# Optimization experiments

Measured on AMD Instinct MI355X. Metric: run time of the kernel, lower is better.

The kernel has to match this reference:

```python
import jax, jax.numpy as jnp
import numpy as np

LAG = 5
MSG_HID = 256
N_ATOMS = 30
N_EDGES = N_ATOMS * (N_ATOMS - 1)  # 870
BATCH = 2
T = 200


def _rel_matrices():
    # fully-connected directed graph, no self loops (standard NRI encoding)
    recv, send = [], []
    for i in range(N_ATOMS):
        for j in range(N_ATOMS):
            if i != j:
                recv.append(i)
                send.append(j)
    rel_rec = np.zeros((N_EDGES, N_ATOMS), dtype=np.float32)
    rel_send = np.zeros((N_EDGES, N_ATOMS), dtype=np.float32)
    rel_rec[np.arange(N_EDGES), recv] = 1.0
    rel_send[np.arange(N_EDGES), send] = 1.0
    return jnp.asarray(rel_rec), jnp.asarray(rel_send)


def setup_inputs() -> dict:
    key = jax.random.key(0)
    ks = jax.random.split(key, 14)
    rel_rec, rel_send = _rel_matrices()
    s = 0.05
    return {
        "inputs": jax.random.normal(ks[0], (BATCH, N_ATOMS, T), jnp.float32),
        "mu": jax.random.normal(ks[1], (BATCH, N_EDGES), jnp.float32),
        "logvar": jax.random.normal(ks[2], (BATCH, N_EDGES), jnp.float32) * 0.1,
        "eps": jax.random.normal(ks[3], (BATCH, N_EDGES), jnp.float32),
        "rel_rec": rel_rec,
        "rel_send": rel_send,
        "w_msg1": jax.random.normal(ks[4], (2 * LAG, MSG_HID), jnp.float32) * s,
        "b_msg1": jnp.zeros((MSG_HID,), jnp.float32),
        "w_msg2": jax.random.normal(ks[5], (MSG_HID, MSG_HID), jnp.float32) * s,
        "b_msg2": jnp.zeros((MSG_HID,), jnp.float32),
        "w_out1": jax.random.normal(ks[6], (LAG + MSG_HID, MSG_HID), jnp.float32) * s,
        "b_out1": jnp.zeros((MSG_HID,), jnp.float32),
        "w_out2": jax.random.normal(ks[7], (MSG_HID, MSG_HID), jnp.float32) * s,
        "b_out2": jnp.zeros((MSG_HID,), jnp.float32),
        "w_out3": jax.random.normal(ks[8], (MSG_HID, 1), jnp.float32) * s,
        "b_out3": jnp.zeros((1,), jnp.float32),
    }


def reference(inputs, mu, logvar, eps, rel_rec, rel_send,
              w_msg1, b_msg1, w_msg2, b_msg2,
              w_out1, b_out1, w_out2, b_out2, w_out3, b_out3):
    # reparametrize: edges [B, E]
    edges = eps * jnp.exp(0.5 * logvar) + mu

    # lag-stack: data [B, T-lag, N, lag]
    Tm = inputs.shape[2] - LAG
    data = jnp.stack([inputs[:, :, i:i + Tm] for i in range(LAG)], axis=-1)
    data = jnp.transpose(data, (0, 2, 1, 3))  # [B, Tm, N, lag]

    # gather node features to edges via one-hot matmuls
    receivers = jnp.einsum('en,btnl->btel', rel_rec, data)   # [B, Tm, E, lag]
    senders = jnp.einsum('en,btnl->btel', rel_send, data)    # [B, Tm, E, lag]
    pre_msg = jnp.concatenate([senders, receivers], axis=-1)  # [B, Tm, E, 2*lag]

    msg = jax.nn.relu(pre_msg @ w_msg1 + b_msg1)
    msg = jax.nn.relu(msg @ w_msg2 + b_msg2)                 # [B, Tm, E, hid]
    msg = msg * edges[:, None, :, None]                       # edge mask

    # scatter-aggregate messages back to receiver nodes
    agg_msgs = jnp.einsum('bteh,en->btnh', msg, rel_rec)      # [B, Tm, N, hid]

    aug = jnp.concatenate([data, agg_msgs], axis=-1)          # [B, Tm, N, lag+hid]
    pred = jax.nn.relu(aug @ w_out1 + b_out1)
    pred = jax.nn.relu(pred @ w_out2 + b_out2)
    pred = (pred @ w_out3 + b_out3)[..., 0]                   # [B, Tm, N]

    return jnp.transpose(pred, (0, 2, 1))                     # [B, N, Tm]
```

## Files before the change

### kernel.cpp

```cpp
#include <hip/hip_runtime.h>

#define LAG 5
#define HID 256
#define NA 30
#define NE 870
#define TM 195
#define TT 200
#define NB 2
#define EPN 29
#define TB3 65
#define NROWS (NB * TM * NA)
#define APAD 4
#define KC 32
#define UVB 1463
#define W2F_ELEMS (HID * HID)
#define W1F_ELEMS (HID * 288)

typedef _Float16 f16;
typedef _Float16 f16x8 __attribute__((ext_vector_type(8)));
typedef float floatx4 __attribute__((ext_vector_type(4)));

__global__ __launch_bounds__(256) void k1_prep(
    const float* __restrict__ inputs, const float* __restrict__ w_msg1,
    const float* __restrict__ b_msg1, const float* __restrict__ w_msg2,
    const float* __restrict__ w_out1, const float* __restrict__ w_out2,
    f16* __restrict__ u, f16* __restrict__ v, f16* __restrict__ w2frag,
    f16* __restrict__ w1frag, f16* __restrict__ w2ofrag)
{
    const int bid = blockIdx.x, tid = threadIdx.x;
    if (bid < UVB) {
        __shared__ float feats8[8][LAG];
        const int r0 = bid * 8;
        if (tid < 8 * LAG) {
            const int i = tid / LAG, l = tid % LAG;
            const int r = r0 + i;
            float fv = 0.f;
            if (r < NROWS) {
                const int b = r / (TM * NA), rem = r % (TM * NA);
                const int t = rem / NA, n = rem % NA;
                fv = inputs[(b * NA + n) * TT + t + l];
            }
            feats8[i][l] = fv;
        }
        float w1c[2 * LAG];
        #pragma unroll
        for (int k = 0; k < 2 * LAG; ++k) w1c[k] = w_msg1[k * HID + tid];
        const float bb = b_msg1[tid];
        __syncthreads();
        #pragma unroll
        for (int i = 0; i < 8; ++i) {
            const int r = r0 + i;
            if (r < NROWS) {
                float ua = bb, va = 0.f;
                #pragma unroll
                for (int l = 0; l < LAG; ++l) {
                    ua = fmaf(feats8[i][l], w1c[l], ua);
                    va = fmaf(feats8[i][l], w1c[LAG + l], va);
                }
                u[(r << 8) + tid] = (f16)ua;
                v[(r << 8) + tid] = (f16)va;
            }
        }
    } else if (bid < UVB + 32) {
        const int fidx = (bid - UVB) * 256 + tid;
        const int lane = fidx & 63;
        const int kc = (fidx >> 6) & 7;
        const int ntc = fidx >> 9;
        const int col = ntc * 16 + (lane & 15);
        const int kb = kc * KC + (lane >> 4) * 8;
        f16x8 vv;
        #pragma unroll
        for (int x = 0; x < 8; ++x) vv[x] = (f16)w_msg2[(kb + x) * HID + col];
        *(f16x8*)&w2frag[fidx * 8] = vv;
    } else if (bid < UVB + 32 + 36) {
        const int fidx = (bid - (UVB + 32)) * 256 + tid;
        const int lane = fidx & 63;
        const int kc = (fidx >> 6) % 9;
        const int ntc = fidx / (64 * 9);
        const int col = ntc * 16 + (lane & 15);
        const int kb = kc * KC + (lane >> 4) * 8;
        f16x8 vv;
        #pragma unroll
        for (int x = 0; x < 8; ++x) {
            const int k = kb + x;
            float val;
            if (k < 256)      val = w_out1[(5 + k) * HID + col];
            else if (k < 261) val = w_out1[(k - 256) * HID + col];
            else              val = 0.f;
            vv[x] = (f16)val;
        }
        *(f16x8*)&w1frag[fidx * 8] = vv;
    } else {
        const int fidx = (bid - (UVB + 32 + 36)) * 256 + tid;
        const int lane = fidx & 63;
        const int kc = (fidx >> 6) & 7;
        const int ntc = fidx >> 9;
        const int col = ntc * 16 + (lane & 15);
        const int kb = kc * KC + (lane >> 4) * 8;
        f16x8 vv;
        #pragma unroll
        for (int x = 0; x < 8; ++x) vv[x] = (f16)w_msg2[0] * (f16)0.f + (f16)w_out2[(kb + x) * HID + col];
        *(f16x8*)&w2ofrag[fidx * 8] = vv;
    }
}

__global__ __launch_bounds__(512, 4) void k2_msg(
    const f16* __restrict__ u, const f16* __restrict__ v,
    const f16* __restrict__ w2frag,
    const float* __restrict__ mu, const float* __restrict__ logvar,
    const float* __restrict__ eps, const float* __restrict__ b_msg2,
    f16* __restrict__ agg)
{
    __shared__ f16 a_lds[96][HID + APAD];
    __shared__ float ev_lds[32];

    const int bid = blockIdx.x;
    const int n  = bid % NA;
    const int tb = (bid / NA) % TB3;
    const int b  = bid / (NA * TB3);
    const int t0 = tb * 3;
    const int tid = threadIdx.x;
    const int lane = tid & 63, w = tid >> 6;
    const int q = lane >> 4, m15 = lane & 15;
    const int wbase = w * 32;

    if (tid < 32) {
        float evv = 0.f;
        if (tid < EPN) {
            const int e = b * NE + n * EPN + tid;
            evv = eps[e] * __expf(0.5f * logvar[e]) + mu[e];
        }
        ev_lds[tid] = evv;
    }

    const f16x8 z8 = {(f16)0, (f16)0, (f16)0, (f16)0, (f16)0, (f16)0, (f16)0, (f16)0};

    #pragma unroll
    for (int i = 0; i < 6; ++i) {
        const int task = i * 512 + tid;
        const int row = task >> 5, c = task & 31;
        const int tt = row >> 5, ei = row & 31;
        f16x8 out8;
        if (ei < EPN) {
            const int t = t0 + tt;
            const int j = ei + (ei >= n);
            const f16x8 uu = *(const f16x8*)(u + ((((b * TM + t) * NA + j) << 8) + c * 8));
            const f16x8 vv = *(const f16x8*)(v + ((((b * TM + t) * NA + n) << 8) + c * 8));
            out8 = __builtin_elementwise_max(uu + vv, z8);
        } else {
            out8 = z8;
        }
        *(f16x8*)&a_lds[row][c * 8] = out8;
    }

    const f16* bbase = w2frag + (lane << 3);
    f16x8 b0[2], b1[2], b2[2];
    #pragma unroll
    for (int nt = 0; nt < 2; ++nt) {
        b0[nt] = *(const f16x8*)(bbase + (((w * 2 + nt) * 8 + 0) << 9));
        b1[nt] = *(const f16x8*)(bbase + (((w * 2 + nt) * 8 + 1) << 9));
    }

    floatx4 acc[6][2];
    #pragma unroll
    for (int mt = 0; mt < 6; ++mt)
        #pragma unroll
        for (int nt = 0; nt < 2; ++nt)
            acc[mt][nt] = (floatx4){0.f, 0.f, 0.f, 0.f};

    __syncthreads();

    #pragma unroll
    for (int kc = 0; kc < 8; ++kc) {
        if (kc < 6) {
            #pragma unroll
            for (int nt = 0; nt < 2; ++nt)
                b2[nt] = *(const f16x8*)(bbase + (((w * 2 + nt) * 8 + kc + 2) << 9));
        }
        f16x8 af[6];
        #pragma unroll
        for (int mt = 0; mt < 6; ++mt)
            af[mt] = *(const f16x8*)&a_lds[mt * 16 + m15][kc * KC + q * 8];
        #pragma unroll
        for (int nt = 0; nt < 2; ++nt)
            #pragma unroll
            for (int mt = 0; mt < 6; ++mt)
                acc[mt][nt] = __builtin_amdgcn_mfma_f32_16x16x32_f16(af[mt], b0[nt], acc[mt][nt], 0, 0, 0);
        #pragma unroll
        for (int nt = 0; nt < 2; ++nt) { b0[nt] = b1[nt]; b1[nt] = b2[nt]; }
    }

    float b2v[2];
    #pragma unroll
    for (int nt = 0; nt < 2; ++nt) b2v[nt] = b_msg2[wbase + nt * 16 + m15];

    #pragma unroll
    for (int tt = 0; tt < 3; ++tt) {
        const int t = t0 + tt;
        #pragma unroll
        for (int nt = 0; nt < 2; ++nt) {
            float part = 0.f;
            #pragma unroll
            for (int ml = 0; ml < 2; ++ml) {
                const int mt = tt * 2 + ml;
                #pragma unroll
                for (int reg = 0; reg < 4; ++reg) {
                    const int ei = (ml * 16 + q * 4 + reg);
                    part += ev_lds[ei] * fmaxf(acc[mt][nt][reg] + b2v[nt], 0.f);
                }
            }
            part += __shfl_xor(part, 16, 64);
            part += __shfl_xor(part, 32, 64);
            if (q == 0)
                agg[((((b * TM + t) * NA + n) << 8) + wbase + nt * 16 + m15)] = (f16)part;
        }
    }
}

__global__ __launch_bounds__(256) void k3_out(
    const f16* __restrict__ agg, const float* __restrict__ inputs,
    const f16* __restrict__ w1frag, const f16* __restrict__ w2ofrag,
    const float* __restrict__ b_out1, const float* __restrict__ b_out2,
    const float* __restrict__ w_out3, const float* __restrict__ b_out3,
    float* __restrict__ out)
{
    __shared__ f16 a1[16][288 + APAD];
    __shared__ float red[4][16];

    const int R0 = blockIdx.x * 16;
    const int tid = threadIdx.x;
    const int lane = tid & 63, w = tid >> 6;
    const int q = lane >> 4, m15 = lane & 15;
    const int wbase = w * 64;

    #pragma unroll
    for (int i = 0; i < 2; ++i) {
        const int task = i * 256 + tid;
        const int row = task >> 5, c = task & 31;
        const int R = R0 + row;
        f16x8 val;
        if (R < NROWS) {
            val = *(const f16x8*)&agg[(R << 8) + c * 8];
        } else {
            for (int x = 0; x < 8; ++x) val[x] = (f16)0.f;
        }
        *(f16x8*)&a1[row][c * 8] = val;
    }
    if (tid < 16) {
        const int R = R0 + tid;
        if (R < NROWS) {
            const int b = R / (TM * NA), rem = R % (TM * NA);
            const int t = rem / NA, n = rem % NA;
            const float* ip = inputs + (b * NA + n) * TT + t;
            #pragma unroll
            for (int l = 0; l < LAG; ++l) a1[tid][256 + l] = (f16)ip[l];
            #pragma unroll
            for (int k = 261; k < 288; ++k) a1[tid][k] = (f16)0.f;
        } else {
            for (int k = 256; k < 288; ++k) a1[tid][k] = (f16)0.f;
        }
    }

    floatx4 acc[4];
    #pragma unroll
    for (int nt = 0; nt < 4; ++nt) acc[nt] = (floatx4){0.f, 0.f, 0.f, 0.f};

    const f16* b1base = w1frag + (lane << 3);
    f16x8 bcur[4], bnxt[4];
    #pragma unroll
    for (int nt = 0; nt < 4; ++nt)
        bcur[nt] = *(const f16x8*)(b1base + (((w * 4 + nt) * 9 + 0) << 9));

    __syncthreads();

    #pragma unroll
    for (int kc = 0; kc < 9; ++kc) {
        if (kc < 8) {
            #pragma unroll
            for (int nt = 0; nt < 4; ++nt)
                bnxt[nt] = *(const f16x8*)(b1base + (((w * 4 + nt) * 9 + kc + 1) << 9));
        }
        const f16x8 af = *(const f16x8*)&a1[m15][kc * KC + q * 8];
        #pragma unroll
        for (int nt = 0; nt < 4; ++nt)
            acc[nt] = __builtin_amdgcn_mfma_f32_16x16x32_f16(af, bcur[nt], acc[nt], 0, 0, 0);
        #pragma unroll
        for (int nt = 0; nt < 4; ++nt) bcur[nt] = bnxt[nt];
    }
    __syncthreads();

    {
        float b1v[4];
        #pragma unroll
        for (int nt = 0; nt < 4; ++nt) b1v[nt] = b_out1[wbase + nt * 16 + m15];
        #pragma unroll
        for (int nt = 0; nt < 4; ++nt)
            #pragma unroll
            for (int reg = 0; reg < 4; ++reg)
                a1[q * 4 + reg][wbase + nt * 16 + m15] =
                    (f16)fmaxf(acc[nt][reg] + b1v[nt], 0.f);
    }

    #pragma unroll
    for (int nt = 0; nt < 4; ++nt) acc[nt] = (floatx4){0.f, 0.f, 0.f, 0.f};

    const f16* b2base = w2ofrag + (lane << 3);
    #pragma unroll
    for (int nt = 0; nt < 4; ++nt)
        bcur[nt] = *(const f16x8*)(b2base + (((w * 4 + nt) * 8 + 0) << 9));

    __syncthreads();

    #pragma unroll
    for (int kc = 0; kc < 8; ++kc) {
        if (kc < 7) {
            #pragma unroll
            for (int nt = 0; nt < 4; ++nt)
                bnxt[nt] = *(const f16x8*)(b2base + (((w * 4 + nt) * 8 + kc + 1) << 9));
        }
        const f16x8 af = *(const f16x8*)&a1[m15][kc * KC + q * 8];
        #pragma unroll
        for (int nt = 0; nt < 4; ++nt)
            acc[nt] = __builtin_amdgcn_mfma_f32_16x16x32_f16(af, bcur[nt], acc[nt], 0, 0, 0);
        #pragma unroll
        for (int nt = 0; nt < 4; ++nt) bcur[nt] = bnxt[nt];
    }

    {
        float b2v[4], w3v[4];
        #pragma unroll
        for (int nt = 0; nt < 4; ++nt) {
            const int col = wbase + nt * 16 + m15;
            b2v[nt] = b_out2[col];
            w3v[nt] = w_out3[col];
        }
        #pragma unroll
        for (int reg = 0; reg < 4; ++reg) {
            float p = 0.f;
            #pragma unroll
            for (int nt = 0; nt < 4; ++nt)
                p += fmaxf(acc[nt][reg] + b2v[nt], 0.f) * w3v[nt];
            p += __shfl_xor(p, 1, 64);
            p += __shfl_xor(p, 2, 64);
            p += __shfl_xor(p, 4, 64);
            p += __shfl_xor(p, 8, 64);
            if (m15 == 0) red[w][q * 4 + reg] = p;
        }
    }
    __syncthreads();
    if (tid < 16) {
        const int R = R0 + tid;
        if (R < NROWS) {
            const float val = red[0][tid] + red[1][tid] + red[2][tid] + red[3][tid] + b_out3[0];
            const int b = R / (TM * NA), rem = R % (TM * NA);
            const int t = rem / NA, n = rem % NA;
            out[(b * NA + n) * TM + t] = val;
        }
    }
}

extern "C" void kernel_launch(void* const* d_in, const int* in_sizes, int n_in,
                              void* d_out, int out_size, void* d_ws, size_t ws_size,
                              hipStream_t stream) {
    const float* inputs  = (const float*)d_in[0];
    const float* mu      = (const float*)d_in[1];
    const float* logvar  = (const float*)d_in[2];
    const float* eps     = (const float*)d_in[3];
    const float* w_msg1  = (const float*)d_in[6];
    const float* b_msg1  = (const float*)d_in[7];
    const float* w_msg2  = (const float*)d_in[8];
    const float* b_msg2  = (const float*)d_in[9];
    const float* w_out1  = (const float*)d_in[10];
    const float* b_out1  = (const float*)d_in[11];
    const float* w_out2  = (const float*)d_in[12];
    const float* b_out2  = (const float*)d_in[13];
    const float* w_out3  = (const float*)d_in[14];
    const float* b_out3  = (const float*)d_in[15];
    float* out = (float*)d_out;

    f16* u       = (f16*)d_ws;
    f16* v       = u       + NROWS * HID;
    f16* aggw    = v       + NROWS * HID;
    f16* w2frag  = aggw    + NROWS * HID;
    f16* w1frag  = w2frag  + W2F_ELEMS;
    f16* w2ofrag = w1frag  + W1F_ELEMS;

    hipLaunchKernelGGL(k1_prep, dim3(UVB + 32 + 36 + 32), dim3(256), 0, stream,
                       inputs, w_msg1, b_msg1, w_msg2, w_out1, w_out2,
                       u, v, w2frag, w1frag, w2ofrag);
    hipLaunchKernelGGL(k2_msg, dim3(NB * NA * TB3), dim3(512), 0, stream,
                       u, v, w2frag, mu, logvar, eps, b_msg2, aggw);
    hipLaunchKernelGGL(k3_out, dim3((NROWS + 15) / 16), dim3(256), 0, stream,
                       aggw, inputs, w1frag, w2ofrag, b_out1, b_out2, w_out3, b_out3, out);
}
```

Measured before the change: 156.4 us.

## Make message kernel persistent with double-buffered LDS tiles and register-resident weights

The message-MLP kernel becomes persistent: a fixed grid of 256 blocks loops over all 3900 tiles. Each block keeps its full W2 fragment set in registers and double-buffers the A tile in dynamic LDS. The next tile's u/v rows and edge parameters are loaded into registers while the MFMA loop runs on the current tile, then written to the other buffer. The aim is to cut per-block launch overhead and repeated weight loads, and to hide global-load latency behind compute. The cost is more registers (occupancy drops to 2 waves/SIMD), larger LDS, and only 256 blocks on a 256-CU device, so load balance depends on tile counts.

```diff
diff --git a/kernel.cpp b/kernel.cpp
--- a/kernel.cpp
+++ b/kernel.cpp
@@ -15,6 +15,11 @@
 #define UVB 1463
 #define W2F_ELEMS (HID * HID)
 #define W1F_ELEMS (HID * 288)
+#define NTILES (NB * NA * TB3)
+#define K2GRID 256
+#define AROW (HID + APAD)
+#define ABUF (96 * AROW)
+#define K2_LDS_BYTES (2 * ABUF * 2 + 2 * 32 * 4)
 
 typedef _Float16 f16;
 typedef _Float16 f16x8 __attribute__((ext_vector_type(8)));
@@ -104,116 +109,173 @@
     }
 }
 
-__global__ __launch_bounds__(512, 4) void k2_msg(
+__global__ __launch_bounds__(512, 2) void k2_msg(
     const f16* __restrict__ u, const f16* __restrict__ v,
     const f16* __restrict__ w2frag,
     const float* __restrict__ mu, const float* __restrict__ logvar,
     const float* __restrict__ eps, const float* __restrict__ b_msg2,
     f16* __restrict__ agg)
 {
-    __shared__ f16 a_lds[96][HID + APAD];
-    __shared__ float ev_lds[32];
-
-    const int bid = blockIdx.x;
-    const int n  = bid % NA;
-    const int tb = (bid / NA) % TB3;
-    const int b  = bid / (NA * TB3);
-    const int t0 = tb * 3;
+    extern __shared__ f16 smem[];
+    float* evb = (float*)(smem + 2 * ABUF);
+
     const int tid = threadIdx.x;
     const int lane = tid & 63, w = tid >> 6;
     const int q = lane >> 4, m15 = lane & 15;
     const int wbase = w * 32;
-
-    if (tid < 32) {
-        float evv = 0.f;
+    const int tid5 = tid >> 5;
+    const int cc = (tid & 31) * 8;
+
+    f16x8 bfr[2][8];
+    #pragma unroll
+    for (int nt = 0; nt < 2; ++nt)
+        #pragma unroll
+        for (int kc = 0; kc < 8; ++kc)
+            bfr[nt][kc] = *(const f16x8*)(w2frag + ((((w * 2 + nt) * 8 + kc) << 9) + (lane << 3)));
+
+    float b2v[2];
+    #pragma unroll
+    for (int nt = 0; nt < 2; ++nt) b2v[nt] = b_msg2[wbase + nt * 16 + m15];
+
+    const f16x8 z8 = {(f16)0, (f16)0, (f16)0, (f16)0, (f16)0, (f16)0, (f16)0, (f16)0};
+
+    int tile = blockIdx.x;
+    int cn = tile % NA;
+    int cr = tile / NA;
+    int ct0 = (cr % TB3) * 3, cb = cr / TB3;
+
+    f16x8 su[6], sv[3];
+    float r_eps = 0.f, r_lv = 0.f, r_mu = 0.f;
+
+    {
+        const int sbase = (cb * TM + ct0) * NA;
+        const int j_e = tid5 + (tid5 >= cn);
+        const int j_o = 16 + tid5 + ((16 + tid5) >= cn);
+        #pragma unroll
+        for (int i = 0; i < 6; ++i) {
+            const int ttt = i >> 1;
+            if (!(i & 1))
+                su[i] = *(const f16x8*)(u + (((sbase + ttt * NA + j_e) << 8) + cc));
+            else if (tid5 < 13)
+                su[i] = *(const f16x8*)(u + (((sbase + ttt * NA + j_o) << 8) + cc));
+        }
+        #pragma unroll
+        for (int ttt = 0; ttt < 3; ++ttt)
+            sv[ttt] = *(const f16x8*)(v + (((sbase + ttt * NA + cn) << 8) + cc));
         if (tid < EPN) {
-            const int e = b * NE + n * EPN + tid;
-            evv = eps[e] * __expf(0.5f * logvar[e]) + mu[e];
-        }
-        ev_lds[tid] = evv;
-    }
-
-    const f16x8 z8 = {(f16)0, (f16)0, (f16)0, (f16)0, (f16)0, (f16)0, (f16)0, (f16)0};
-
-    #pragma unroll
-    for (int i = 0; i < 6; ++i) {
-        const int task = i * 512 + tid;
-        const int row = task >> 5, c = task & 31;
-        const int tt = row >> 5, ei = row & 31;
-        f16x8 out8;
-        if (ei < EPN) {
-            const int t = t0 + tt;
-            const int j = ei + (ei >= n);
-            const f16x8 uu = *(const f16x8*)(u + ((((b * TM + t) * NA + j) << 8) + c * 8));
-            const f16x8 vv = *(const f16x8*)(v + ((((b * TM + t) * NA + n) << 8) + c * 8));
-            out8 = __builtin_elementwise_max(uu + vv, z8);
-        } else {
-            out8 = z8;
-        }
-        *(f16x8*)&a_lds[row][c * 8] = out8;
-    }
-
-    const f16* bbase = w2frag + (lane << 3);
-    f16x8 b0[2], b1[2], b2[2];
-    #pragma unroll
-    for (int nt = 0; nt < 2; ++nt) {
-        b0[nt] = *(const f16x8*)(bbase + (((w * 2 + nt) * 8 + 0) << 9));
-        b1[nt] = *(const f16x8*)(bbase + (((w * 2 + nt) * 8 + 1) << 9));
-    }
-
-    floatx4 acc[6][2];
-    #pragma unroll
-    for (int mt = 0; mt < 6; ++mt)
-        #pragma unroll
-        for (int nt = 0; nt < 2; ++nt)
-            acc[mt][nt] = (floatx4){0.f, 0.f, 0.f, 0.f};
-
-    __syncthreads();
-
-    #pragma unroll
-    for (int kc = 0; kc < 8; ++kc) {
-        if (kc < 6) {
+            const int e = cb * NE + cn * EPN + tid;
+            r_eps = eps[e]; r_lv = logvar[e]; r_mu = mu[e];
+        }
+        #pragma unroll
+        for (int i = 0; i < 6; ++i) {
+            f16x8 out8 = z8;
+            if (!(i & 1) || tid5 < 13)
+                out8 = __builtin_elementwise_max(su[i] + sv[i >> 1], z8);
+            *(f16x8*)(smem + (i * 16 + tid5) * AROW + cc) = out8;
+        }
+        if (tid < 32) {
+            float evv = 0.f;
+            if (tid < EPN) evv = r_eps * __expf(0.5f * r_lv) + r_mu;
+            evb[tid] = evv;
+        }
+    }
+
+    int cur = 0;
+    for (;;) {
+        const int nxt = tile + K2GRID;
+        const bool have = (nxt < NTILES);
+        int nn = 0, nt0 = 0, nb = 0;
+
+        __syncthreads();
+
+        if (have) {
+            nn = nxt % NA;
+            const int nr = nxt / NA;
+            nt0 = (nr % TB3) * 3; nb = nr / TB3;
+            const int sbase = (nb * TM + nt0) * NA;
+            const int j_e = tid5 + (tid5 >= nn);
+            const int j_o = 16 + tid5 + ((16 + tid5) >= nn);
+            #pragma unroll
+            for (int i = 0; i < 6; ++i) {
+                const int ttt = i >> 1;
+                if (!(i & 1))
+                    su[i] = *(const f16x8*)(u + (((sbase + ttt * NA + j_e) << 8) + cc));
+                else if (tid5 < 13)
+                    su[i] = *(const f16x8*)(u + (((sbase + ttt * NA + j_o) << 8) + cc));
+            }
+            #pragma unroll
+            for (int ttt = 0; ttt < 3; ++ttt)
+                sv[ttt] = *(const f16x8*)(v + (((sbase + ttt * NA + nn) << 8) + cc));
+            if (tid < EPN) {
+                const int e = nb * NE + nn * EPN + tid;
+                r_eps = eps[e]; r_lv = logvar[e]; r_mu = mu[e];
+            }
+        }
+
+        floatx4 acc[6][2];
+        #pragma unroll
+        for (int mt = 0; mt < 6; ++mt)
             #pragma unroll
             for (int nt = 0; nt < 2; ++nt)
-                b2[nt] = *(const f16x8*)(bbase + (((w * 2 + nt) * 8 + kc + 2) << 9));
-        }
-        f16x8 af[6];
-        #pragma unroll
-        for (int mt = 0; mt < 6; ++mt)
-            af[mt] = *(const f16x8*)&a_lds[mt * 16 + m15][kc * KC + q * 8];
-        #pragma unroll
-        for (int nt = 0; nt < 2; ++nt)
+                acc[mt][nt] = (floatx4){0.f, 0.f, 0.f, 0.f};
+
+        const f16* abuf = smem + cur * ABUF;
+        __builtin_amdgcn_s_setprio(1);
+        #pragma unroll
+        for (int kc = 0; kc < 8; ++kc) {
+            f16x8 af[6];
             #pragma unroll
             for (int mt = 0; mt < 6; ++mt)
-                acc[mt][nt] = __builtin_amdgcn_mfma_f32_16x16x32_f16(af[mt], b0[nt], acc[mt][nt], 0, 0, 0);
-        #pragma unroll
-        for (int nt = 0; nt < 2; ++nt) { b0[nt] = b1[nt]; b1[nt] = b2[nt]; }
-    }
-
-    float b2v[2];
-    #pragma unroll
-    for (int nt = 0; nt < 2; ++nt) b2v[nt] = b_msg2[wbase + nt * 16 + m15];
-
-    #pragma unroll
-    for (int tt = 0; tt < 3; ++tt) {
-        const int t = t0 + tt;
-        #pragma unroll
-        for (int nt = 0; nt < 2; ++nt) {
-            float part = 0.f;
-            #pragma unroll
-            for (int ml = 0; ml < 2; ++ml) {
-                const int mt = tt * 2 + ml;
+                af[mt] = *(const f16x8*)(abuf + (mt * 16 + m15) * AROW + kc * KC + q * 8);
+            #pragma unroll
+            for (int nt = 0; nt < 2; ++nt)
                 #pragma unroll
-                for (int reg = 0; reg < 4; ++reg) {
-                    const int ei = (ml * 16 + q * 4 + reg);
-                    part += ev_lds[ei] * fmaxf(acc[mt][nt][reg] + b2v[nt], 0.f);
+                for (int mt = 0; mt < 6; ++mt)
+                    acc[mt][nt] = __builtin_amdgcn_mfma_f32_16x16x32_f16(af[mt], bfr[nt][kc], acc[mt][nt], 0, 0, 0);
+        }
+        __builtin_amdgcn_s_setprio(0);
+
+        if (have) {
+            f16* nbuf = smem + (cur ^ 1) * ABUF;
+            #pragma unroll
+            for (int i = 0; i < 6; ++i) {
+                f16x8 out8 = z8;
+                if (!(i & 1) || tid5 < 13)
+                    out8 = __builtin_elementwise_max(su[i] + sv[i >> 1], z8);
+                *(f16x8*)(nbuf + (i * 16 + tid5) * AROW + cc) = out8;
+            }
+            if (tid < 32) {
+                float evv = 0.f;
+                if (tid < EPN) evv = r_eps * __expf(0.5f * r_lv) + r_mu;
+                evb[(cur ^ 1) * 32 + tid] = evv;
+            }
+        }
+
+        const float* ev = evb + cur * 32;
+        #pragma unroll
+        for (int tt = 0; tt < 3; ++tt) {
+            const int t = ct0 + tt;
+            #pragma unroll
+            for (int nt = 0; nt < 2; ++nt) {
+                float part = 0.f;
+                #pragma unroll
+                for (int ml = 0; ml < 2; ++ml) {
+                    const int mt = tt * 2 + ml;
+                    #pragma unroll
+                    for (int reg = 0; reg < 4; ++reg) {
+                        const int ei = ml * 16 + q * 4 + reg;
+                        part += ev[ei] * fmaxf(acc[mt][nt][reg] + b2v[nt], 0.f);
+                    }
                 }
-            }
-            part += __shfl_xor(part, 16, 64);
-            part += __shfl_xor(part, 32, 64);
-            if (q == 0)
-                agg[((((b * TM + t) * NA + n) << 8) + wbase + nt * 16 + m15)] = (f16)part;
-        }
+                part += __shfl_xor(part, 16, 64);
+                part += __shfl_xor(part, 32, 64);
+                if (q == 0)
+                    agg[((((cb * TM + t) * NA + cn) << 8) + wbase + nt * 16 + m15)] = (f16)part;
+            }
+        }
+
+        if (!have) break;
+        tile = nxt; cn = nn; ct0 = nt0; cb = nb; cur ^= 1;
     }
 }
 
@@ -385,10 +447,18 @@
     f16* w1frag  = w2frag  + W2F_ELEMS;
     f16* w2ofrag = w1frag  + W1F_ELEMS;
 
+    static int k2_attr_done = 0;
+    if (!k2_attr_done) {
+        hipFuncSetAttribute(reinterpret_cast<const void*>(k2_msg),
+                            hipFuncAttributeMaxDynamicSharedMemorySize,
+                            (int)K2_LDS_BYTES);
+        k2_attr_done = 1;
+    }
+
     hipLaunchKernelGGL(k1_prep, dim3(UVB + 32 + 36 + 32), dim3(256), 0, stream,
                        inputs, w_msg1, b_msg1, w_msg2, w_out1, w_out2,
                        u, v, w2frag, w1frag, w2ofrag);
-    hipLaunchKernelGGL(k2_msg, dim3(NB * NA * TB3), dim3(512), 0, stream,
+    hipLaunchKernelGGL(k2_msg, dim3(K2GRID), dim3(512), K2_LDS_BYTES, stream,
                        u, v, w2frag, mu, logvar, eps, b_msg2, aggw);
     hipLaunchKernelGGL(k3_out, dim3((NROWS + 15) / 16), dim3(256), 0, stream,
                        aggw, inputs, w1frag, w2ofrag, b_out1, b_out2, w_out3, b_out3, out);
```

Result: slower. 310.5 us (+98.6%).

## Switch message GEMM to 32x32x16 MFMA with swizzled LDS and 256-thread blocks

Applied to the files above, without the earlier changes.

Rewrites the k2 message kernel to use 32x32x16 f16 MFMA tiles in place of 16x16x32. Each of four waves now covers 64 output columns instead of eight waves covering 32. The w_msg2 fragment layout is repacked to match, and the padded LDS tile is replaced by an XOR-swizzled layout to avoid bank conflicts. The goal is fewer MFMA and LDS-read instructions and a cheaper reduction, at the cost of more accumulator registers per thread and fewer threads per block. It also removes a dead multiply in the w_out2 packing.

```diff
diff --git a/kernel.cpp b/kernel.cpp
--- a/kernel.cpp
+++ b/kernel.cpp
@@ -19,6 +19,7 @@
 typedef _Float16 f16;
 typedef _Float16 f16x8 __attribute__((ext_vector_type(8)));
 typedef float floatx4 __attribute__((ext_vector_type(4)));
+typedef float floatx16 __attribute__((ext_vector_type(16)));
 
 __global__ __launch_bounds__(256) void k1_prep(
     const float* __restrict__ inputs, const float* __restrict__ w_msg1,
@@ -64,10 +65,10 @@
     } else if (bid < UVB + 32) {
         const int fidx = (bid - UVB) * 256 + tid;
         const int lane = fidx & 63;
-        const int kc = (fidx >> 6) & 7;
-        const int ntc = fidx >> 9;
-        const int col = ntc * 16 + (lane & 15);
-        const int kb = kc * KC + (lane >> 4) * 8;
+        const int kc = (fidx >> 6) & 15;
+        const int c32 = fidx >> 10;
+        const int col = c32 * 32 + (lane & 31);
+        const int kb = kc * 16 + (lane >> 5) * 8;
         f16x8 vv;
         #pragma unroll
         for (int x = 0; x < 8; ++x) vv[x] = (f16)w_msg2[(kb + x) * HID + col];
@@ -99,19 +100,19 @@
         const int kb = kc * KC + (lane >> 4) * 8;
         f16x8 vv;
         #pragma unroll
-        for (int x = 0; x < 8; ++x) vv[x] = (f16)w_msg2[0] * (f16)0.f + (f16)w_out2[(kb + x) * HID + col];
+        for (int x = 0; x < 8; ++x) vv[x] = (f16)w_out2[(kb + x) * HID + col];
         *(f16x8*)&w2ofrag[fidx * 8] = vv;
     }
 }
 
-__global__ __launch_bounds__(512, 4) void k2_msg(
+__global__ __launch_bounds__(256, 3) void k2_msg(
     const f16* __restrict__ u, const f16* __restrict__ v,
     const f16* __restrict__ w2frag,
     const float* __restrict__ mu, const float* __restrict__ logvar,
     const float* __restrict__ eps, const float* __restrict__ b_msg2,
     f16* __restrict__ agg)
 {
-    __shared__ f16 a_lds[96][HID + APAD];
+    __shared__ f16 a_lds[96 * 256];
     __shared__ float ev_lds[32];
 
     const int bid = blockIdx.x;
@@ -121,8 +122,7 @@
     const int t0 = tb * 3;
     const int tid = threadIdx.x;
     const int lane = tid & 63, w = tid >> 6;
-    const int q = lane >> 4, m15 = lane & 15;
-    const int wbase = w * 32;
+    const int h = lane >> 5, l31 = lane & 31;
 
     if (tid < 32) {
         float evv = 0.f;
@@ -135,84 +135,83 @@
 
     const f16x8 z8 = {(f16)0, (f16)0, (f16)0, (f16)0, (f16)0, (f16)0, (f16)0, (f16)0};
 
-    #pragma unroll
-    for (int i = 0; i < 6; ++i) {
-        const int task = i * 512 + tid;
+    const int sbase = (b * TM + t0) * NA;
+    #pragma unroll
+    for (int i = 0; i < 12; ++i) {
+        const int task = i * 256 + tid;
         const int row = task >> 5, c = task & 31;
         const int tt = row >> 5, ei = row & 31;
-        f16x8 out8;
+        f16x8 out8 = z8;
         if (ei < EPN) {
-            const int t = t0 + tt;
             const int j = ei + (ei >= n);
-            const f16x8 uu = *(const f16x8*)(u + ((((b * TM + t) * NA + j) << 8) + c * 8));
-            const f16x8 vv = *(const f16x8*)(v + ((((b * TM + t) * NA + n) << 8) + c * 8));
+            const f16x8 uu = *(const f16x8*)(u + (((sbase + tt * NA + j) << 8) + c * 8));
+            const f16x8 vv = *(const f16x8*)(v + (((sbase + tt * NA + n) << 8) + c * 8));
             out8 = __builtin_elementwise_max(uu + vv, z8);
-        } else {
-            out8 = z8;
-        }
-        *(f16x8*)&a_lds[row][c * 8] = out8;
+        }
+        *(f16x8*)&a_lds[row * 256 + ((c * 8) ^ ((row & 7) << 3))] = out8;
     }
 
     const f16* bbase = w2frag + (lane << 3);
     f16x8 b0[2], b1[2], b2[2];
     #pragma unroll
     for (int nt = 0; nt < 2; ++nt) {
-        b0[nt] = *(const f16x8*)(bbase + (((w * 2 + nt) * 8 + 0) << 9));
-        b1[nt] = *(const f16x8*)(bbase + (((w * 2 + nt) * 8 + 1) << 9));
-    }
-
-    floatx4 acc[6][2];
-    #pragma unroll
-    for (int mt = 0; mt < 6; ++mt)
+        const int c32 = w * 2 + nt;
+        b0[nt] = *(const f16x8*)(bbase + (((c32 * 16) + 0) << 9));
+        b1[nt] = *(const f16x8*)(bbase + (((c32 * 16) + 1) << 9));
+    }
+
+    floatx16 acc[3][2];
+    #pragma unroll
+    for (int mt = 0; mt < 3; ++mt)
         #pragma unroll
         for (int nt = 0; nt < 2; ++nt)
-            acc[mt][nt] = (floatx4){0.f, 0.f, 0.f, 0.f};
-
-    __syncthreads();
-
-    #pragma unroll
-    for (int kc = 0; kc < 8; ++kc) {
-        if (kc < 6) {
+            #pragma unroll
+            for (int x = 0; x < 16; ++x) acc[mt][nt][x] = 0.f;
+
+    __syncthreads();
+
+    #pragma unroll
+    for (int kc = 0; kc < 16; ++kc) {
+        if (kc < 14) {
             #pragma unroll
             for (int nt = 0; nt < 2; ++nt)
-                b2[nt] = *(const f16x8*)(bbase + (((w * 2 + nt) * 8 + kc + 2) << 9));
-        }
-        f16x8 af[6];
-        #pragma unroll
-        for (int mt = 0; mt < 6; ++mt)
-            af[mt] = *(const f16x8*)&a_lds[mt * 16 + m15][kc * KC + q * 8];
+                b2[nt] = *(const f16x8*)(bbase + ((((w * 2 + nt) * 16) + kc + 2) << 9));
+        }
+        f16x8 af[3];
+        #pragma unroll
+        for (int mt = 0; mt < 3; ++mt) {
+            const int row = mt * 32 + l31;
+            af[mt] = *(const f16x8*)&a_lds[row * 256 + ((kc * 16 + h * 8) ^ ((row & 7) << 3))];
+        }
         #pragma unroll
         for (int nt = 0; nt < 2; ++nt)
             #pragma unroll
-            for (int mt = 0; mt < 6; ++mt)
-                acc[mt][nt] = __builtin_amdgcn_mfma_f32_16x16x32_f16(af[mt], b0[nt], acc[mt][nt], 0, 0, 0);
+            for (int mt = 0; mt < 3; ++mt)
+                acc[mt][nt] = __builtin_amdgcn_mfma_f32_32x32x16_f16(af[mt], b0[nt], acc[mt][nt], 0, 0, 0);
         #pragma unroll
         for (int nt = 0; nt < 2; ++nt) { b0[nt] = b1[nt]; b1[nt] = b2[nt]; }
     }
 
-    float b2v[2];
-    #pragma unroll
-    for (int nt = 0; nt < 2; ++nt) b2v[nt] = b_msg2[wbase + nt * 16 + m15];
-
-    #pragma unroll
-    for (int tt = 0; tt < 3; ++tt) {
-        const int t = t0 + tt;
+    float evr[16];
+    #pragma unroll
+    for (int reg = 0; reg < 16; ++reg)
+        evr[reg] = ev_lds[(reg & 3) + 8 * (reg >> 2) + 4 * h];
+    float b2s[2];
+    #pragma unroll
+    for (int nt = 0; nt < 2; ++nt) b2s[nt] = b_msg2[w * 64 + nt * 32 + l31];
+
+    #pragma unroll
+    for (int mt = 0; mt < 3; ++mt) {
+        const int t = t0 + mt;
         #pragma unroll
         for (int nt = 0; nt < 2; ++nt) {
             float part = 0.f;
             #pragma unroll
-            for (int ml = 0; ml < 2; ++ml) {
-                const int mt = tt * 2 + ml;
-                #pragma unroll
-                for (int reg = 0; reg < 4; ++reg) {
-                    const int ei = (ml * 16 + q * 4 + reg);
-                    part += ev_lds[ei] * fmaxf(acc[mt][nt][reg] + b2v[nt], 0.f);
-                }
-            }
-            part += __shfl_xor(part, 16, 64);
+            for (int reg = 0; reg < 16; ++reg)
+                part += evr[reg] * fmaxf(acc[mt][nt][reg] + b2s[nt], 0.f);
             part += __shfl_xor(part, 32, 64);
-            if (q == 0)
-                agg[((((b * TM + t) * NA + n) << 8) + wbase + nt * 16 + m15)] = (f16)part;
+            if (h == 0)
+                agg[(((b * TM + t) * NA + n) << 8) + w * 64 + nt * 32 + l31] = (f16)part;
         }
     }
 }
@@ -388,7 +387,7 @@
     hipLaunchKernelGGL(k1_prep, dim3(UVB + 32 + 36 + 32), dim3(256), 0, stream,
                        inputs, w_msg1, b_msg1, w_msg2, w_out1, w_out2,
                        u, v, w2frag, w1frag, w2ofrag);
-    hipLaunchKernelGGL(k2_msg, dim3(NB * NA * TB3), dim3(512), 0, stream,
+    hipLaunchKernelGGL(k2_msg, dim3(NB * NA * TB3), dim3(256), 0, stream,
                        u, v, w2frag, mu, logvar, eps, b_msg2, aggw);
     hipLaunchKernelGGL(k3_out, dim3((NROWS + 15) / 16), dim3(256), 0, stream,
                        aggw, inputs, w1frag, w2ofrag, b_out1, b_out2, w_out3, b_out3, out);
```

Measured after the change: 162.8 us. 4.1% more time.
